# Kernel tuning notes

Measured on AMD Instinct MI355X. Metric: run time of the kernel, lower is better.

Reference implementation:

```python
import jax, jax.numpy as jnp
import numpy as np

N = 50000
E = 800000
IN = 256
OUT = 32
H1 = 8
NEG_SLOPE = 0.2


def setup_inputs() -> dict:
    key = jax.random.key(0)
    ks = jax.random.split(key, 12)
    x = jax.random.normal(ks[0], (N, IN), dtype=jnp.float32)
    src = jax.random.randint(ks[1], (E,), 0, N, dtype=jnp.int32)
    dst = jax.random.randint(ks[2], (E,), 0, N, dtype=jnp.int32)
    s1 = 1.0 / np.sqrt(IN)
    s2 = 1.0 / np.sqrt(H1 * OUT)
    # layer 1 (8 heads, residual = Identity since IN == H1*OUT)
    W1 = jax.random.normal(ks[3], (IN, H1 * OUT), dtype=jnp.float32) * s1
    al1 = jax.random.normal(ks[4], (H1, OUT), dtype=jnp.float32) * s1
    ar1 = jax.random.normal(ks[5], (H1, OUT), dtype=jnp.float32) * s1
    b1 = jnp.zeros((H1 * OUT,), dtype=jnp.float32)
    # layer 2 (1 head, residual = Linear since H1*OUT != OUT)
    W2 = jax.random.normal(ks[6], (H1 * OUT, OUT), dtype=jnp.float32) * s2
    al2 = jax.random.normal(ks[7], (1, OUT), dtype=jnp.float32) * s2
    ar2 = jax.random.normal(ks[8], (1, OUT), dtype=jnp.float32) * s2
    resW2 = jax.random.normal(ks[9], (H1 * OUT, OUT), dtype=jnp.float32) * s2
    b2 = jnp.zeros((OUT,), dtype=jnp.float32)
    return {"x": x, "src": src, "dst": dst, "W1": W1, "al1": al1, "ar1": ar1,
            "b1": b1, "W2": W2, "al2": al2, "ar2": ar2, "resW2": resW2, "b2": b2}


def gat_layer(x, src, dst, W, al, ar, bias, heads, out_feats, res_fn):
    # x: (N, in). feat: (N, H, D)
    feat = (x @ W).reshape(N, heads, out_feats)
    el = jnp.sum(feat * al[None], axis=-1)  # (N, H)
    er = jnp.sum(feat * ar[None], axis=-1)  # (N, H)
    e = jax.nn.leaky_relu(el[src] + er[dst], NEG_SLOPE)  # (E, H)
    # edge softmax over incoming edges of each destination node
    emax = jax.ops.segment_max(e, dst, num_segments=N)  # (N, H)
    ee = jnp.exp(e - emax[dst])
    esum = jax.ops.segment_sum(ee, dst, num_segments=N)  # (N, H)
    a = ee / esum[dst]  # (E, H)
    # gather-multiply-scatter-add aggregation
    msg = feat[src] * a[..., None]  # (E, H, D)
    rst = jax.ops.segment_sum(msg, dst, num_segments=N)  # (N, H, D)
    rst = rst + res_fn(x)
    rst = rst + bias.reshape(1, heads, out_feats)
    return rst


def reference(x, src, dst, W1, al1, ar1, b1, W2, al2, ar2, resW2, b2):
    # layer 1: 8 heads, residual Identity (IN == H1*OUT)
    y = gat_layer(x, src, dst, W1, al1, ar1, b1, H1, OUT,
                  lambda h: h.reshape(N, H1, OUT))
    y = jax.nn.relu(y).reshape(N, H1 * OUT)
    # layer 2: 1 head, residual Linear projection
    y = gat_layer(y, src, dst, W2, al2, ar2, b2, 1, OUT,
                  lambda h: (h @ resW2).reshape(N, 1, OUT))
    return y
```

## Files before the change

### kernel.cpp

```cpp
#include <hip/hip_runtime.h>
#include <hip/hip_bf16.h>
#include <hip/hip_fp8.h>

#define N_NODES 50000
#define M_PAD   50048
#define N_EDGES 800000
#define NEG_SLOPE 0.2f

#define EPT 8
#define BKA 391
#define NBUCK 256
#define NPB 196
#define SEGCAP 40
#define GHALF 782
#define MEGA1_T (BKA + GHALF)
#define MEGA1_PRIME 577ull
#define MEGA2_T (NBUCK + GHALF)
#define MEGA2_PRIME 521ull

typedef __attribute__((ext_vector_type(8))) short bf16x8;
typedef __attribute__((ext_vector_type(4))) float f32x4;
typedef __attribute__((ext_vector_type(2))) float f32x2;

__device__ __forceinline__ unsigned short f2bf(float f) {
    unsigned u = __float_as_uint(f);
    u += 0x7FFFu + ((u >> 16) & 1u);
    return (unsigned short)(u >> 16);
}
__device__ __forceinline__ float bf2f(unsigned short h) {
    return __uint_as_float(((unsigned)h) << 16);
}

#if __has_builtin(__builtin_amdgcn_cvt_pk_f32_fp8)
__device__ __forceinline__ f32x2 fp8pk_lo(unsigned int p) { return __builtin_amdgcn_cvt_pk_f32_fp8(p, false); }
__device__ __forceinline__ f32x2 fp8pk_hi(unsigned int p) { return __builtin_amdgcn_cvt_pk_f32_fp8(p, true); }
#else
__device__ __forceinline__ float fp82f_s(unsigned char b) {
    __hip_fp8_e4m3 t; t.__x = (__hip_fp8_storage_t)b; return (float)t;
}
__device__ __forceinline__ f32x2 fp8pk_lo(unsigned int p) {
    f32x2 r; r.x = fp82f_s(p & 0xff); r.y = fp82f_s((p >> 8) & 0xff); return r;
}
__device__ __forceinline__ f32x2 fp8pk_hi(unsigned int p) {
    f32x2 r; r.x = fp82f_s((p >> 16) & 0xff); r.y = fp82f_s(p >> 24); return r;
}
#endif

#if __has_builtin(__builtin_amdgcn_cvt_pk_fp8_f32)
__device__ __forceinline__ unsigned int fp8enc2(float a, float b) {
    return (unsigned int)__builtin_amdgcn_cvt_pk_fp8_f32(a, b, 0, false);
}
#else
__device__ __forceinline__ unsigned int fp8enc2(float a, float b) {
    __hip_fp8_e4m3 ta(a), tb(b);
    return (unsigned int)ta.__x | ((unsigned int)tb.__x << 8);
}
#endif


__global__ __launch_bounds__(256) void k_trans(const float* __restrict__ W1, const float* __restrict__ W2,
                                               const float* __restrict__ resW2, const float* __restrict__ x,
                                               unsigned short* __restrict__ W1T, unsigned short* __restrict__ W2T,
                                               unsigned short* __restrict__ xb, unsigned int* __restrict__ btot) {
    int flat = blockIdx.y * 10 + blockIdx.x;
    if (flat == 0) btot[threadIdx.x] = 0;

    if (blockIdx.y < 8) {
        __shared__ unsigned short tile[32][33];
        int bx = blockIdx.x;
        const float* in;
        unsigned short* out;
        int Nn, n0;
        if (bx < 8)      { in = W1;    out = W1T;            Nn = 256; n0 = bx * 32; }
        else if (bx == 8){ in = W2;    out = W2T;            Nn = 32;  n0 = 0; }
        else             { in = resW2; out = W2T + 32 * 256; Nn = 32;  n0 = 0; }
        int k0 = blockIdx.y * 32;
        int tx = threadIdx.x & 31, ty = threadIdx.x >> 5;
        #pragma unroll
        for (int r = 0; r < 4; ++r) {
            int k = k0 + ty + r * 8;
            tile[ty + r * 8][tx] = f2bf(in[(size_t)k * Nn + n0 + tx]);
        }
        __syncthreads();
        #pragma unroll
        for (int r = 0; r < 4; ++r) {
            int n = ty + r * 8;
            out[(size_t)(n0 + n) * 256 + k0 + tx] = tile[tx][n];
        }
    } else {
        int xid = flat - 80;
        const size_t NCHUNK = (size_t)M_PAD * 256 / 8;
        for (size_t c = (size_t)xid * 256 + threadIdx.x; c < NCHUNK; c += (size_t)720 * 256) {
            size_t base = c * 8;
            float4 a = make_float4(0.f, 0.f, 0.f, 0.f), b = a;
            if (base < (size_t)N_NODES * 256) {
                a = *(const float4*)(x + base);
                b = *(const float4*)(x + base + 4);
            }
            ushort4 h0, h1;
            h0.x = f2bf(a.x); h0.y = f2bf(a.y); h0.z = f2bf(a.z); h0.w = f2bf(a.w);
            h1.x = f2bf(b.x); h1.y = f2bf(b.y); h1.z = f2bf(b.z); h1.w = f2bf(b.w);
            *(ushort4*)(xb + base) = h0;
            *(ushort4*)(xb + base + 4) = h1;
        }
    }
}


__device__ __forceinline__ void gemm1_half(int g, int bn0,
                                           const unsigned short* __restrict__ xb,
                                           const unsigned short* __restrict__ BT,
                                           const float* __restrict__ al1, const float* __restrict__ ar1,
                                           unsigned char* __restrict__ Cb8,
                                           float* __restrict__ el1, float* __restrict__ er1) {
    const int t = threadIdx.x;
    const int bm0 = g * 64;
    const int wave = t >> 6, lane = t & 63;
    const int wm = (wave & 1) * 32, wn = (wave >> 1) * 64;
    const int lm = lane & 15, quad = lane >> 4;

    f32x4 acc[2][4];
    #pragma unroll
    for (int i = 0; i < 2; ++i)
        #pragma unroll
        for (int j = 0; j < 4; ++j)
            #pragma unroll
            for (int r = 0; r < 4; ++r) acc[i][j][r] = 0.f;

    const unsigned short* bp[4];
    const unsigned short* ap[2];
    #pragma unroll
    for (int i = 0; i < 4; ++i)
        bp[i] = BT + (size_t)(bn0 + wn + i * 16 + lm) * 256 + quad * 8;
    #pragma unroll
    for (int i = 0; i < 2; ++i)
        ap[i] = xb + (size_t)(bm0 + wm + i * 16 + lm) * 256 + quad * 8;

    bf16x8 nb[4], na[2];
    #pragma unroll
    for (int i = 0; i < 4; ++i) nb[i] = *(const bf16x8*)(bp[i]);
    #pragma unroll
    for (int i = 0; i < 2; ++i) na[i] = *(const bf16x8*)(ap[i]);

    #pragma unroll
    for (int k0 = 0; k0 < 256; k0 += 32) {
        bf16x8 cb[4], ca[2];
        #pragma unroll
        for (int i = 0; i < 4; ++i) cb[i] = nb[i];
        #pragma unroll
        for (int i = 0; i < 2; ++i) ca[i] = na[i];
        if (k0 + 32 < 256) {
            #pragma unroll
            for (int i = 0; i < 4; ++i) nb[i] = *(const bf16x8*)(bp[i] + k0 + 32);
            #pragma unroll
            for (int i = 0; i < 2; ++i) na[i] = *(const bf16x8*)(ap[i] + k0 + 32);
        }
        #pragma unroll
        for (int mi = 0; mi < 2; ++mi)
            #pragma unroll
            for (int ni = 0; ni < 4; ++ni)
                acc[mi][ni] = __builtin_amdgcn_mfma_f32_16x16x32_bf16(ca[mi], cb[ni], acc[mi][ni], 0, 0, 0);
    }

    #pragma unroll
    for (int mi = 0; mi < 2; ++mi) {
        #pragma unroll
        for (int ni = 0; ni < 4; ++ni) {
            int col = bn0 + wn + ni * 16 + lm;
            int row0 = bm0 + wm + mi * 16 + quad * 4;
            unsigned int p01 = fp8enc2(acc[mi][ni][0], acc[mi][ni][1]);
            unsigned int p23 = fp8enc2(acc[mi][ni][2], acc[mi][ni][3]);
            Cb8[(size_t)(row0 + 0) * 256 + col] = (unsigned char)(p01 & 0xff);
            Cb8[(size_t)(row0 + 1) * 256 + col] = (unsigned char)((p01 >> 8) & 0xff);
            Cb8[(size_t)(row0 + 2) * 256 + col] = (unsigned char)(p23 & 0xff);
            Cb8[(size_t)(row0 + 3) * 256 + col] = (unsigned char)((p23 >> 8) & 0xff);
        }
    }
    float alv[4], arv[4];
    #pragma unroll
    for (int ni = 0; ni < 4; ++ni) {
        int colg = bn0 + wn + ni * 16 + lm;
        alv[ni] = al1[colg];
        arv[ni] = ar1[colg];
    }
    int head0 = (bn0 + wn) >> 5;
    #pragma unroll
    for (int gg = 0; gg < 2; ++gg) {
        #pragma unroll
        for (int mi = 0; mi < 2; ++mi) {
            #pragma unroll
            for (int r = 0; r < 4; ++r) {
                float pel = acc[mi][2 * gg][r] * alv[2 * gg] + acc[mi][2 * gg + 1][r] * alv[2 * gg + 1];
                float per = acc[mi][2 * gg][r] * arv[2 * gg] + acc[mi][2 * gg + 1][r] * arv[2 * gg + 1];
                #pragma unroll
                for (int m = 1; m <= 8; m <<= 1) {
                    pel += __shfl_xor(pel, m, 64);
                    per += __shfl_xor(per, m, 64);
                }
                if (lm == 0) {
                    int row = bm0 + wm + mi * 16 + quad * 4 + r;
                    el1[row * 8 + head0 + gg] = pel;
                    er1[row * 8 + head0 + gg] = per;
                }
            }
        }
    }
}


__global__ __launch_bounds__(256) void k_mega1(const int* __restrict__ src, const int* __restrict__ dst,
                                               uint2* __restrict__ seg, unsigned int* __restrict__ cnt,
                                               unsigned int* __restrict__ btot,
                                               const unsigned short* __restrict__ xb,
                                               const unsigned short* __restrict__ BT,
                                               const float* __restrict__ al1, const float* __restrict__ ar1,
                                               unsigned char* __restrict__ Cb8,
                                               float* __restrict__ el1, float* __restrict__ er1) {
    __shared__ unsigned int lcnt[NBUCK];
    unsigned vb = (unsigned)(((unsigned long long)blockIdx.x * MEGA1_PRIME) % MEGA1_T);
    if (vb < BKA) {
        lcnt[threadIdx.x] = 0;
        __syncthreads();
        int base = vb * (256 * EPT) + threadIdx.x;
        int sv[EPT], dv[EPT], bk[EPT], lr[EPT];
        #pragma unroll
        for (int q = 0; q < EPT; ++q) {
            int i = base + q * 256;
            if (i < N_EDGES) { sv[q] = src[i]; dv[q] = dst[i]; }
            else dv[q] = -1;
        }
        #pragma unroll
        for (int q = 0; q < EPT; ++q) {
            if (dv[q] >= 0) {
                bk[q] = (int)((unsigned)dv[q] / NPB);
                lr[q] = atomicAdd(&lcnt[bk[q]], 1u);
            }
        }
        __syncthreads();
        cnt[vb * NBUCK + threadIdx.x] = lcnt[threadIdx.x];
        if (lcnt[threadIdx.x] > 0) atomicAdd(&btot[threadIdx.x], lcnt[threadIdx.x]);
        #pragma unroll
        for (int q = 0; q < EPT; ++q) {
            if (dv[q] >= 0 && lr[q] < SEGCAP) {
                size_t slot = ((size_t)bk[q] * BKA + vb) * SEGCAP + lr[q];
                seg[slot] = make_uint2((unsigned)sv[q], (unsigned)dv[q] - (unsigned)bk[q] * NPB);
            }
        }
        return;
    }
    gemm1_half(vb - BKA, 0, xb, BT, al1, ar1, Cb8, el1, er1);
}


__global__ __launch_bounds__(256) void k_mega2(const uint2* __restrict__ seg, const unsigned int* __restrict__ cnt,
                                               const unsigned int* __restrict__ btot,
                                               int* __restrict__ rowoff, int* __restrict__ csr_src,
                                               const unsigned short* __restrict__ xb,
                                               const unsigned short* __restrict__ BT,
                                               const float* __restrict__ al1, const float* __restrict__ ar1,
                                               unsigned char* __restrict__ Cb8,
                                               float* __restrict__ el1, float* __restrict__ er1) {
    __shared__ unsigned int hist[NPB];
    __shared__ unsigned int cursor[NPB];
    __shared__ unsigned int red[256];
    unsigned vb = (unsigned)(((unsigned long long)blockIdx.x * MEGA2_PRIME) % MEGA2_T);
    if (vb < NBUCK) {
        int b = (int)vb;
        int t = threadIdx.x;
        if (t < NPB) hist[t] = 0;
        red[t] = (t < b) ? btot[t] : 0;
        __syncthreads();
        #pragma unroll
        for (int off = 128; off > 0; off >>= 1) {
            if (t < off) red[t] += red[t + off];
            __syncthreads();
        }
        unsigned int base = red[0];
        __syncthreads();
        for (int s = t; s < BKA; s += 256) {
            unsigned int c = cnt[s * NBUCK + b];
            const uint2* sp = seg + ((size_t)b * BKA + s) * SEGCAP;
            for (unsigned int j = 0; j < c; ++j) {
                atomicAdd(&hist[sp[j].y], 1u);
            }
        }
        __syncthreads();
        red[t] = (t < NPB) ? hist[t] : 0;
        __syncthreads();
        for (int off = 1; off < 256; off <<= 1) {
            unsigned int val = (t >= off) ? red[t - off] : 0;
            __syncthreads();
            red[t] += val;
            __syncthreads();
        }
        if (t < NPB) {
            unsigned int excl = red[t] - hist[t];
            cursor[t] = excl;
            int v = b * NPB + t;
            if (v < N_NODES) rowoff[v] = (int)(base + excl);
        }
        if (b == NBUCK - 1 && t == 0) rowoff[N_NODES] = N_EDGES;
        __syncthreads();
        for (int s = t; s < BKA; s += 256) {
            unsigned int c = cnt[s * NBUCK + b];
            const uint2* sp = seg + ((size_t)b * BKA + s) * SEGCAP;
            for (unsigned int j = 0; j < c; ++j) {
                uint2 eg = sp[j];
                unsigned int r = atomicAdd(&cursor[eg.y], 1u);
                csr_src[base + r] = (int)eg.x;
            }
        }
        return;
    }
    gemm1_half(vb - NBUCK, 128, xb, BT, al1, ar1, Cb8, el1, er1);
}


__global__ __launch_bounds__(256) void k_agg1(const unsigned char* __restrict__ feat8,
                                              const float* __restrict__ el1, const float* __restrict__ er1,
                                              const unsigned short* __restrict__ xb, const float* __restrict__ b1,
                                              const int* __restrict__ rowoff, const int* __restrict__ csr_src,
                                              unsigned short* __restrict__ y_b) {
    int v = (blockIdx.x * 256 + threadIdx.x) >> 6;
    int lane = threadIdx.x & 63;
    if (v >= M_PAD) return;
    int c0 = lane * 4;
    if (v >= N_NODES) {
        ushort4 z = {0, 0, 0, 0};
        *(ushort4*)(y_b + (size_t)v * 256 + c0) = z;
        return;
    }
    int h = lane >> 3;
    float er  = er1[v * 8 + h];
    float erc = er1[v * 8 + (lane & 7)];
    float ax = 0.f, ay = 0.f, az = 0.f, aw = 0.f, wsum = 0.f;
    int s = rowoff[v], e = rowoff[v + 1];
    int j = s;
    for (; j + 7 < e; j += 8) {
        int um = csr_src[j + (lane >> 3)];
        float elv = el1[um * 8 + (lane & 7)];
        int u[8];
        #pragma unroll
        for (int q = 0; q < 8; ++q) u[q] = __shfl(um, q * 8);
        unsigned int hv[8];
        #pragma unroll
        for (int q = 0; q < 8; ++q) hv[q] = *(const unsigned int*)(feat8 + (size_t)u[q] * 256 + c0);
        float tq = elv + erc;
        tq = fmaxf(tq, NEG_SLOPE * tq);
        float wv = __expf(tq);
        #pragma unroll
        for (int q = 0; q < 8; ++q) {
            float w = __shfl(wv, q * 8 + h);
            wsum += w;
            f32x2 lo = fp8pk_lo(hv[q]);
            f32x2 hi = fp8pk_hi(hv[q]);
            ax += w * lo.x; ay += w * lo.y; az += w * hi.x; aw += w * hi.y;
        }
    }
    for (; j + 3 < e; j += 4) {
        int u[4];
        #pragma unroll
        for (int q = 0; q < 4; ++q) u[q] = csr_src[j + q];
        float tt[4];
        #pragma unroll
        for (int q = 0; q < 4; ++q) tt[q] = el1[u[q] * 8 + h] + er;
        unsigned int hv[4];
        #pragma unroll
        for (int q = 0; q < 4; ++q) hv[q] = *(const unsigned int*)(feat8 + (size_t)u[q] * 256 + c0);
        #pragma unroll
        for (int q = 0; q < 4; ++q) {
            float tq = fmaxf(tt[q], NEG_SLOPE * tt[q]);
            float w = __expf(tq);
            wsum += w;
            f32x2 lo = fp8pk_lo(hv[q]);
            f32x2 hi = fp8pk_hi(hv[q]);
            ax += w * lo.x; ay += w * lo.y; az += w * hi.x; aw += w * hi.y;
        }
    }
    for (; j < e; ++j) {
        int u = csr_src[j];
        float t = el1[u * 8 + h] + er;
        unsigned int hh = *(const unsigned int*)(feat8 + (size_t)u * 256 + c0);
        t = fmaxf(t, NEG_SLOPE * t);
        float w = __expf(t);
        wsum += w;
        f32x2 lo = fp8pk_lo(hh);
        f32x2 hi = fp8pk_hi(hh);
        ax += w * lo.x; ay += w * lo.y; az += w * hi.x; aw += w * hi.y;
    }
    float inv = (e > s) ? 1.f / wsum : 0.f;
    ushort4 rh = *(const ushort4*)(xb + (size_t)v * 256 + c0);
    float4 bb = *(const float4*)(b1 + c0);
    ushort4 o;
    o.x = f2bf(fmaxf(ax * inv + bf2f(rh.x) + bb.x, 0.f));
    o.y = f2bf(fmaxf(ay * inv + bf2f(rh.y) + bb.y, 0.f));
    o.z = f2bf(fmaxf(az * inv + bf2f(rh.z) + bb.z, 0.f));
    o.w = f2bf(fmaxf(aw * inv + bf2f(rh.w) + bb.w, 0.f));
    *(ushort4*)(y_b + (size_t)v * 256 + c0) = o;
}


__global__ __launch_bounds__(256) void k_gemm2f(const unsigned short* __restrict__ Ab,
                                                const unsigned short* __restrict__ BT,
                                                const float* __restrict__ al2, const float* __restrict__ ar2,
                                                unsigned short* __restrict__ feat2b, float* __restrict__ res2,
                                                float* __restrict__ el2, float* __restrict__ er2) {
    const int t = threadIdx.x;
    const int bm0 = blockIdx.x * 64;
    const int wave = t >> 6, lane = t & 63;
    const int wm = (wave & 1) * 32, wn = (wave >> 1) * 32;
    const int lm = lane & 15, quad = lane >> 4;

    f32x4 acc[2][2];
    #pragma unroll
    for (int i = 0; i < 2; ++i)
        #pragma unroll
        for (int j = 0; j < 2; ++j)
            #pragma unroll
            for (int r = 0; r < 4; ++r) acc[i][j][r] = 0.f;

    const unsigned short* bp[2];
    const unsigned short* ap[2];
    #pragma unroll
    for (int i = 0; i < 2; ++i) {
        bp[i] = BT + (size_t)(wn + i * 16 + lm) * 256 + quad * 8;
        ap[i] = Ab + (size_t)(bm0 + wm + i * 16 + lm) * 256 + quad * 8;
    }

    bf16x8 nb[2], na[2];
    #pragma unroll
    for (int i = 0; i < 2; ++i) { nb[i] = *(const bf16x8*)(bp[i]); na[i] = *(const bf16x8*)(ap[i]); }

    #pragma unroll
    for (int k0 = 0; k0 < 256; k0 += 32) {
        bf16x8 cb[2], ca[2];
        #pragma unroll
        for (int i = 0; i < 2; ++i) { cb[i] = nb[i]; ca[i] = na[i]; }
        if (k0 + 32 < 256) {
            #pragma unroll
            for (int i = 0; i < 2; ++i) {
                nb[i] = *(const bf16x8*)(bp[i] + k0 + 32);
                na[i] = *(const bf16x8*)(ap[i] + k0 + 32);
            }
        }
        #pragma unroll
        for (int mi = 0; mi < 2; ++mi)
            #pragma unroll
            for (int ni = 0; ni < 2; ++ni)
                acc[mi][ni] = __builtin_amdgcn_mfma_f32_16x16x32_bf16(ca[mi], cb[ni], acc[mi][ni], 0, 0, 0);
    }

    #pragma unroll
    for (int mi = 0; mi < 2; ++mi) {
        #pragma unroll
        for (int ni = 0; ni < 2; ++ni) {
            int col = wn + ni * 16 + lm;
            #pragma unroll
            for (int r = 0; r < 4; ++r) {
                int row = bm0 + wm + mi * 16 + quad * 4 + r;
                float val = acc[mi][ni][r];
                if (col < 32) feat2b[(size_t)row * 32 + col] = f2bf(val);
                else          res2[(size_t)row * 32 + col - 32] = val;
            }
        }
    }
    if (wn == 0) {
        float alv[2], arv[2];
        #pragma unroll
        for (int ni = 0; ni < 2; ++ni) {
            alv[ni] = al2[ni * 16 + lm];
            arv[ni] = ar2[ni * 16 + lm];
        }
        #pragma unroll
        for (int mi = 0; mi < 2; ++mi) {
            #pragma unroll
            for (int r = 0; r < 4; ++r) {
                float pel = acc[mi][0][r] * alv[0] + acc[mi][1][r] * alv[1];
                float per = acc[mi][0][r] * arv[0] + acc[mi][1][r] * arv[1];
                #pragma unroll
                for (int m = 1; m <= 8; m <<= 1) {
                    pel += __shfl_xor(pel, m, 64);
                    per += __shfl_xor(per, m, 64);
                }
                if (lm == 0) {
                    int row = bm0 + wm + mi * 16 + quad * 4 + r;
                    el2[row] = pel;
                    er2[row] = per;
                }
            }
        }
    }
}


__global__ __launch_bounds__(256) void k_agg2(const unsigned short* __restrict__ feat2b,
                                              const float* __restrict__ el2, const float* __restrict__ er2,
                                              const float* __restrict__ res2, const float* __restrict__ b2,
                                              const int* __restrict__ rowoff, const int* __restrict__ csr_src,
                                              float* __restrict__ out) {
    int g = blockIdx.x * 256 + threadIdx.x;
    int v = g >> 5;
    int c = g & 31;
    if (v >= N_NODES) return;
    float er = er2[v];
    float acc = 0.f, wsum = 0.f;
    int s = rowoff[v], e = rowoff[v + 1];
    int j = s;
    for (; j + 3 < e; j += 4) {
        int u[4];
        #pragma unroll
        for (int q = 0; q < 4; ++q) u[q] = csr_src[j + q];
        float tt[4];
        #pragma unroll
        for (int q = 0; q < 4; ++q) tt[q] = el2[u[q]] + er;
        unsigned short fv[4];
        #pragma unroll
        for (int q = 0; q < 4; ++q) fv[q] = feat2b[(size_t)u[q] * 32 + c];
        #pragma unroll
        for (int q = 0; q < 4; ++q) {
            float tq = fmaxf(tt[q], NEG_SLOPE * tt[q]);
            float w = __expf(tq);
            wsum += w;
            acc += w * bf2f(fv[q]);
        }
    }
    for (; j < e; ++j) {
        int u = csr_src[j];
        float t = el2[u] + er;
        t = fmaxf(t, NEG_SLOPE * t);
        float w = __expf(t);
        wsum += w;
        acc += w * bf2f(feat2b[(size_t)u * 32 + c]);
    }
    float inv = (e > s) ? 1.f / wsum : 0.f;
    out[(size_t)v * 32 + c] = acc * inv + res2[(size_t)v * 32 + c] + b2[c];
}


extern "C" void kernel_launch(void* const* d_in, const int* in_sizes, int n_in,
                              void* d_out, int out_size, void* d_ws, size_t ws_size,
                              hipStream_t stream) {
    const float* x     = (const float*)d_in[0];
    const int*   src   = (const int*)d_in[1];
    const int*   dst   = (const int*)d_in[2];
    const float* W1    = (const float*)d_in[3];
    const float* al1   = (const float*)d_in[4];
    const float* ar1   = (const float*)d_in[5];
    const float* b1    = (const float*)d_in[6];
    const float* W2    = (const float*)d_in[7];
    const float* al2   = (const float*)d_in[8];
    const float* ar2   = (const float*)d_in[9];
    const float* resW2 = (const float*)d_in[10];
    const float* b2    = (const float*)d_in[11];
    float* out = (float*)d_out;

    char* ws = (char*)d_ws;
    size_t off = 0;
    auto alloc = [&](size_t bytes) {
        void* p = ws + off;
        off += (bytes + 255) & ~(size_t)255;
        return p;
    };
    unsigned short* xb     = (unsigned short*)alloc((size_t)M_PAD * 256 * 2);
    unsigned char*  feat8  = (unsigned char*)alloc((size_t)M_PAD * 256);
    unsigned short* y_b    = (unsigned short*)alloc((size_t)M_PAD * 256 * 2);
    unsigned short* W1T    = (unsigned short*)alloc((size_t)256 * 256 * 2);
    unsigned short* W2T    = (unsigned short*)alloc((size_t)64 * 256 * 2);
    unsigned short* feat2b = (unsigned short*)alloc((size_t)M_PAD * 32 * 2);
    float* res2   = (float*)alloc((size_t)M_PAD * 32 * 4);
    float* el1    = (float*)alloc((size_t)M_PAD * 8 * 4);
    float* er1    = (float*)alloc((size_t)M_PAD * 8 * 4);
    float* el2    = (float*)alloc((size_t)M_PAD * 4);
    float* er2    = (float*)alloc((size_t)M_PAD * 4);
    int*   rowoff = (int*)alloc((size_t)(N_NODES + 1) * 4);
    int*   csr    = (int*)alloc((size_t)N_EDGES * 4);
    uint2* seg    = (uint2*)alloc((size_t)NBUCK * BKA * SEGCAP * 8);
    unsigned int* cnt  = (unsigned int*)alloc((size_t)BKA * NBUCK * 4);
    unsigned int* btot = (unsigned int*)alloc((size_t)NBUCK * 4);
    (void)ws_size;

    k_trans<<<dim3(10, 80), 256, 0, stream>>>(W1, W2, resW2, x, W1T, W2T, xb, btot);

    k_mega1<<<MEGA1_T, 256, 0, stream>>>(src, dst, seg, cnt, btot, xb, W1T, al1, ar1, feat8, el1, er1);

    k_mega2<<<MEGA2_T, 256, 0, stream>>>(seg, cnt, btot, rowoff, csr, xb, W1T, al1, ar1, feat8, el1, er1);

    k_agg1<<<(M_PAD * 64) / 256, 256, 0, stream>>>(feat8, el1, er1, xb, b1, rowoff, csr, y_b);

    k_gemm2f<<<M_PAD / 64, 256, 0, stream>>>(y_b, W2T, al2, ar2, feat2b, res2, el2, er2);
    k_agg2<<<(N_NODES * 32) / 256, 256, 0, stream>>>(feat2b, el2, er2, res2, b2, rowoff, csr, out);
}
```

Measured before the change: 265.3 us.

## Split agg1 columns into XCD-mapped quarters with 16-lane groups per node

Reworks the layer-1 aggregation so each node's 256 feature columns are split into four 64-column slices. Each slice is handled by a 16-lane group, and the slice index is derived from blockIdx so that the blocks for a given slice land on the same XCD pair. The intent is better L2 locality for the gathered fp8 features and less per-node shuffle overhead. It also drops the 4-edge unrolled tail loop. The cost is four times as many csr/el1 loads per node, and more scalar-loop iterations for edge counts that are not multiples of 8.

```diff
diff --git a/kernel.cpp b/kernel.cpp
--- a/kernel.cpp
+++ b/kernel.cpp
@@ -321,68 +321,53 @@
                                               const unsigned short* __restrict__ xb, const float* __restrict__ b1,
                                               const int* __restrict__ rowoff, const int* __restrict__ csr_src,
                                               unsigned short* __restrict__ y_b) {
-    int v = (blockIdx.x * 256 + threadIdx.x) >> 6;
-    int lane = threadIdx.x & 63;
-    if (v >= M_PAD) return;
-    int c0 = lane * 4;
+    int xcd = blockIdx.x & 7;
+    int s4  = xcd >> 1;
+    int nodeblock = (blockIdx.x >> 3) * 2 + (xcd & 1);
+    int t = threadIdx.x;
+    int g = t >> 4;
+    int l = t & 15;
+    int v = nodeblock * 16 + g;
+    int c0 = s4 * 64 + l * 4;
     if (v >= N_NODES) {
         ushort4 z = {0, 0, 0, 0};
         *(ushort4*)(y_b + (size_t)v * 256 + c0) = z;
         return;
     }
-    int h = lane >> 3;
-    float er  = er1[v * 8 + h];
-    float erc = er1[v * 8 + (lane & 7)];
+    int hb = l >> 3;
+    int h = s4 * 2 + hb;
+    float er = er1[v * 8 + h];
     float ax = 0.f, ay = 0.f, az = 0.f, aw = 0.f, wsum = 0.f;
     int s = rowoff[v], e = rowoff[v + 1];
     int j = s;
+    int gbase = g << 4;
     for (; j + 7 < e; j += 8) {
-        int um = csr_src[j + (lane >> 3)];
-        float elv = el1[um * 8 + (lane & 7)];
-        int u[8];
-        #pragma unroll
-        for (int q = 0; q < 8; ++q) u[q] = __shfl(um, q * 8);
-        unsigned int hv[8];
-        #pragma unroll
-        for (int q = 0; q < 8; ++q) hv[q] = *(const unsigned int*)(feat8 + (size_t)u[q] * 256 + c0);
-        float tq = elv + erc;
+        int um = csr_src[j + (l & 7)];
+        float elv = el1[um * 8 + h];
+        float tq = elv + er;
         tq = fmaxf(tq, NEG_SLOPE * tq);
         float wv = __expf(tq);
+        int u[8];
+        #pragma unroll
+        for (int q = 0; q < 8; ++q) u[q] = __shfl(um, gbase + q);
+        unsigned int hv[8];
+        #pragma unroll
+        for (int q = 0; q < 8; ++q) hv[q] = *(const unsigned int*)(feat8 + (size_t)u[q] * 256 + c0);
         #pragma unroll
         for (int q = 0; q < 8; ++q) {
-            float w = __shfl(wv, q * 8 + h);
+            float w = __shfl(wv, gbase + (hb << 3) + q);
             wsum += w;
             f32x2 lo = fp8pk_lo(hv[q]);
             f32x2 hi = fp8pk_hi(hv[q]);
             ax += w * lo.x; ay += w * lo.y; az += w * hi.x; aw += w * hi.y;
         }
     }
-    for (; j + 3 < e; j += 4) {
-        int u[4];
-        #pragma unroll
-        for (int q = 0; q < 4; ++q) u[q] = csr_src[j + q];
-        float tt[4];
-        #pragma unroll
-        for (int q = 0; q < 4; ++q) tt[q] = el1[u[q] * 8 + h] + er;
-        unsigned int hv[4];
-        #pragma unroll
-        for (int q = 0; q < 4; ++q) hv[q] = *(const unsigned int*)(feat8 + (size_t)u[q] * 256 + c0);
-        #pragma unroll
-        for (int q = 0; q < 4; ++q) {
-            float tq = fmaxf(tt[q], NEG_SLOPE * tt[q]);
-            float w = __expf(tq);
-            wsum += w;
-            f32x2 lo = fp8pk_lo(hv[q]);
-            f32x2 hi = fp8pk_hi(hv[q]);
-            ax += w * lo.x; ay += w * lo.y; az += w * hi.x; aw += w * hi.y;
-        }
-    }
     for (; j < e; ++j) {
         int u = csr_src[j];
-        float t = el1[u * 8 + h] + er;
+        float tt = el1[u * 8 + h] + er;
         unsigned int hh = *(const unsigned int*)(feat8 + (size_t)u * 256 + c0);
-        t = fmaxf(t, NEG_SLOPE * t);
-        float w = __expf(t);
+        tt = fmaxf(tt, NEG_SLOPE * tt);
+        float w = __expf(tt);
         wsum += w;
         f32x2 lo = fp8pk_lo(hh);
         f32x2 hi = fp8pk_hi(hh);
@@ -585,7 +570,7 @@
 
     k_mega2<<<MEGA2_T, 256, 0, stream>>>(seg, cnt, btot, rowoff, csr, xb, W1T, al1, ar1, feat8, el1, er1);
 
-    k_agg1<<<(M_PAD * 64) / 256, 256, 0, stream>>>(feat8, el1, er1, xb, b1, rowoff, csr, y_b);
+    k_agg1<<<12512, 256, 0, stream>>>(feat8, el1, er1, xb, b1, rowoff, csr, y_b);
 
     k_gemm2f<<<M_PAD / 64, 256, 0, stream>>>(y_b, W2T, al2, ar2, feat2b, res2, el2, er2);
     k_agg2<<<(N_NODES * 32) / 256, 256, 0, stream>>>(feat2b, el2, er2, res2, b2, rowoff, csr, out);
```

New measurement: 294.2 us. 10.9% more time.
